# Performance work log

Hardware: AMD Instinct MI355X
Metric: run time of the kernel (lower is better)

The kernel has to match this reference:

```python
import jax, jax.numpy as jnp
import numpy as np

NV = 1_000_000   # number of 'var' nodes
NC = 500_000     # number of 'con' nodes
E = 16_000_000   # number of v2c edges (c2v is the reverse edge set)
H = 10           # n_h_feats


def setup_inputs() -> dict:
    key = jax.random.key(0)
    ks = jax.random.split(key, 24)
    s = 0.1  # weight init scale
    inp = {
        "var_c": jax.random.normal(ks[0], (NV,), jnp.float32),
        "var_x": jax.random.normal(ks[1], (NV,), jnp.float32),
        "con_b": jax.random.normal(ks[2], (NC,), jnp.float32),
        "A": jax.random.uniform(ks[3], (E,), jnp.float32),
        "src": jax.random.randint(ks[4], (E,), 0, NV, jnp.int32),
        "dst": jax.random.randint(ks[5], (E,), 0, NC, jnp.int32),
        # var_emb / con_emb Linear params
        "Wv": jax.random.normal(ks[6], (2, H), jnp.float32) * s,
        "bv": jnp.zeros((H,), jnp.float32),
        "Wc": jax.random.normal(ks[7], (1, H), jnp.float32) * s,
        "bc": jnp.zeros((H,), jnp.float32),
        # conv1 (GraphConv, shared across v2c/c2v) -- note: its output is
        # overwritten in the original forward and never reaches the output
        "W1": jax.random.normal(ks[8], (H, H), jnp.float32) * s,
        "b1": jnp.zeros((H,), jnp.float32),
        # conv2 (GraphConv, shared across v2c/c2v)
        "W2": jax.random.normal(ks[9], (H, H), jnp.float32) * s,
        "b2": jnp.zeros((H,), jnp.float32),
        # output MLP
        "Wo1": jax.random.normal(ks[10], (H, H), jnp.float32) * s,
        "bo1": jnp.zeros((H,), jnp.float32),
        "Wo2": jax.random.normal(ks[11], (H, H), jnp.float32) * s,
        "bo2": jnp.zeros((H,), jnp.float32),
        "Wo3": jax.random.normal(ks[12], (H, 1), jnp.float32) * s,
        "bo3": jnp.zeros((1,), jnp.float32),
    }
    return inp


def _gconv(x_src, W, b, s_idx, d_idx, ew, norm_src, norm_dst, n_dst):
    # DGL GraphConv, norm='both', with edge weights; in==out feats so W first.
    h = (x_src * norm_src) @ W                      # [N_src, H]
    msg = h[s_idx] * ew[:, None]                    # gather + edge weight
    agg = jax.ops.segment_sum(msg, d_idx, num_segments=n_dst)
    return agg * norm_dst + b


def reference(var_c, var_x, con_b, A, src, dst,
              Wv, bv, Wc, bc, W1, b1, W2, b2,
              Wo1, bo1, Wo2, bo2, Wo3, bo3):
    # symmetric norm from UNWEIGHTED degrees (DGL GraphConv norm='both'),
    # clamped at 1. v2c: out-deg(var), in-deg(con); c2v is the reverse.
    ones_e = jnp.ones_like(A)
    deg_v = jnp.clip(jax.ops.segment_sum(ones_e, src, num_segments=NV), 1.0)
    deg_c = jnp.clip(jax.ops.segment_sum(ones_e, dst, num_segments=NC), 1.0)
    norm_v = deg_v[:, None] ** -0.5
    norm_c = deg_c[:, None] ** -0.5

    # node embeddings
    var_feats = jnp.stack([var_c, var_x], axis=1)   # [NV, 2]
    X_var = jax.nn.relu(var_feats @ Wv + bv)        # [NV, H]
    X_con = jax.nn.relu(con_b[:, None] @ Wc + bc)   # [NC, H] (unused by convs: GraphConv ignores dst feats)

    # In the original forward, conv1 outputs (h_con / h_var) are immediately
    # overwritten by conv2 outputs (GraphConv only consumes src features),
    # so only conv2 lies on the effective compute path.
    h_con = jax.nn.relu(_gconv(X_var, W2, b2, src, dst, A, norm_v, norm_c, NC))
    h_var = jax.nn.relu(_gconv(h_con, W2, b2, dst, src, A, norm_c, norm_v, NV))

    h = jax.nn.relu(h_var @ Wo1 + bo1)
    h = jax.nn.relu(h @ Wo2 + bo2)
    logit = h @ Wo3 + bo3                           # [NV, 1]
    # dgl.readout_nodes(op='mean', ntype='var'), single graph -> [1, 1]
    return jnp.mean(logit, axis=0, keepdims=True)
```

## Files before the change

kernel.cpp:

```cpp
#include <hip/hip_runtime.h>

#define HF 10
#define ST 16
#define BST 16
#define SLC 256
#define NBINS 4096
#define NSL 16
#define CAPS 6144


__global__ __launch_bounds__(1024) void k_hist(const int* __restrict__ idx,
                                               unsigned* __restrict__ hist,
                                               long long s_begin, long long s_end, int per) {
    __shared__ unsigned l[NBINS];
    int t = threadIdx.x, sl = blockIdx.x;
    for (int b = t; b < NBINS; b += 1024) l[b] = 0u;
    __syncthreads();
    long long s0 = s_begin + (long long)sl * per;
    long long s1 = s0 + per; if (s1 > s_end) s1 = s_end;
    for (long long i = s0 + t; i < s1; i += 1024)
        atomicAdd(&l[((unsigned)idx[i]) >> 8], 1u);
    __syncthreads();
    unsigned* out = hist + (size_t)sl * NBINS;
    for (int b = t; b < NBINS; b += 1024) out[b] = l[b];
}

__global__ void k_coltot(const unsigned* __restrict__ h, unsigned* __restrict__ colT) {
    int b = blockIdx.x * 256 + threadIdx.x;
    unsigned s = 0u;
    for (int sl = 0; sl < SLC; sl++) s += h[(size_t)sl * NBINS + b];
    colT[b] = s;
}

__global__ __launch_bounds__(1024) void k_prefix(const unsigned* __restrict__ colT,
                                                 unsigned* __restrict__ start) {
    __shared__ unsigned p[1024];
    int t = threadIdx.x;
    uint4 v = *(const uint4*)(colT + 4 * t);
    unsigned own = v.x + v.y + v.z + v.w;
    p[t] = own;
    __syncthreads();
    for (int off = 1; off < 1024; off <<= 1) {
        unsigned u = (t >= off) ? p[t - off] : 0u;
        __syncthreads();
        p[t] += u;
        __syncthreads();
    }
    unsigned e = p[t] - own;
    *(uint4*)(start + 4 * t) = make_uint4(e, e + v.x, e + v.x + v.y, e + v.x + v.y + v.z);
    if (t == 1023) start[NBINS] = p[1023];
}

__global__ void k_offs(unsigned* __restrict__ h, const unsigned* __restrict__ start) {
    int b = blockIdx.x * 256 + threadIdx.x;
    unsigned cur = start[b];
    for (int sl = 0; sl < SLC; sl++) {
        unsigned* cell = h + (size_t)sl * NBINS + b;
        unsigned v = *cell;
        *cell = cur;
        cur += v;
    }
}

__global__ __launch_bounds__(1024) void k_scatS(const int* __restrict__ src, const int* __restrict__ dst,
                                                const float* __restrict__ A,
                                                const unsigned* __restrict__ offs,
                                                uint2* __restrict__ ebufS,
                                                long long E, int per) {
    __shared__ unsigned cur[NBINS];
    int t = threadIdx.x, sl = blockIdx.x;
    const unsigned* o = offs + (size_t)sl * NBINS;
    for (int b = t; b < NBINS; b += 1024) cur[b] = o[b];
    __syncthreads();
    long long s0 = (long long)sl * per;
    long long s1 = s0 + per; if (s1 > E) s1 = E;
    for (long long i = s0 + t; i < s1; i += 1024) {
        unsigned s = (unsigned)src[i], d = (unsigned)dst[i];
        float a = A[i];
        unsigned pos = atomicAdd(&cur[s >> 8], 1u);
        ebufS[pos] = make_uint2(((s & 255u) << 19) | d, __float_as_uint(a));
    }
}

__global__ __launch_bounds__(256) void k_sliceIP(uint2* __restrict__ ebuf,
                                                 const unsigned* __restrict__ startS) {
    __shared__ uint2 ebl[CAPS];
    __shared__ unsigned c16[NSL], p16[NSL];
    int t = threadIdx.x, b = blockIdx.x;
    unsigned i0 = startS[b], i1 = startS[b + 1], n = i1 - i0;
    if (n == 0u || n > (unsigned)CAPS) return;
    if (t < NSL) c16[t] = 0u;
    __syncthreads();
    for (unsigned i = t; i < n; i += 256) {
        uint2 kv = ebuf[i0 + i];
        ebl[i] = kv;
        atomicAdd(&c16[(kv.x & 0x7FFFFu) >> 15], 1u);
    }
    __syncthreads();
    if (t == 0) {
        unsigned run = 0u;
        for (int s = 0; s < NSL; s++) { p16[s] = run; run += c16[s]; }
    }
    __syncthreads();
    for (unsigned i = t; i < n; i += 256) {
        uint2 kv = ebl[i];
        unsigned pos = atomicAdd(&p16[(kv.x & 0x7FFFFu) >> 15], 1u);
        ebuf[i0 + pos] = kv;
    }
}

__global__ void k_cntS2(const uint2* __restrict__ ebufS, const unsigned* __restrict__ startS,
                        const float* __restrict__ var_c, const float* __restrict__ var_x,
                        float4* __restrict__ vcx, int NV) {
    __shared__ unsigned cnt[256];
    int t = threadIdx.x, b = blockIdx.x;
    cnt[t] = 0u;
    __syncthreads();
    unsigned i0 = startS[b], i1 = startS[b + 1];
    for (unsigned i = i0 + t; i < i1; i += 256)
        atomicAdd(&cnt[ebufS[i].x >> 19], 1u);
    __syncthreads();
    int v = b * 256 + t;
    if (v < NV)
        vcx[v] = make_float4(var_c[v], var_x[v], rsqrtf(fmaxf((float)cnt[t], 1.0f)), 0.0f);
}

__global__ __launch_bounds__(1024) void k_histD2(const uint2* __restrict__ ebufB,
                                                 const unsigned* __restrict__ startS,
                                                 unsigned* __restrict__ hist, int B0, int binsPer) {
    __shared__ unsigned l[NBINS];
    int t = threadIdx.x, sl = blockIdx.x;
    for (int b = t; b < NBINS; b += 1024) l[b] = 0u;
    __syncthreads();
    int b0 = B0 + sl * binsPer;
    unsigned i0 = startS[b0], i1 = startS[b0 + binsPer];
    for (unsigned i = i0 + t; i < i1; i += 1024)
        atomicAdd(&l[(ebufB[i].x & 0x7FFFFu) >> 8], 1u);
    __syncthreads();
    unsigned* out = hist + (size_t)sl * NBINS;
    for (int b = t; b < NBINS; b += 1024) out[b] = l[b];
}

__global__ __launch_bounds__(1024) void k_scatD2(const uint2* __restrict__ ebufB,
                                                 const unsigned* __restrict__ startS,
                                                 const unsigned* __restrict__ offs,
                                                 const float4* __restrict__ vcx,
                                                 uint4* __restrict__ ebufD, int B0, int binsPer,
                                                 unsigned cap) {
    __shared__ unsigned cur[NBINS];
    int t = threadIdx.x, sl = blockIdx.x;
    const unsigned* o = offs + (size_t)sl * NBINS;
    for (int b = t; b < NBINS; b += 1024) cur[b] = o[b];
    __syncthreads();
    int b0 = B0 + sl * binsPer;
    for (int bb = 0; bb < binsPer; bb++) {
        int bin = b0 + bb;
        unsigned vbase = ((unsigned)bin) << 8;
        unsigned i0 = startS[bin], i1 = startS[bin + 1];
        for (unsigned i = i0 + t; i < i1; i += 1024) {
            uint2 kv = ebufB[i];
            unsigned d = kv.x & 0x7FFFFu;
            float4 g = vcx[vbase | (kv.x >> 19)];
            unsigned pos = atomicAdd(&cur[d >> 8], 1u);
            if (pos < cap)
                ebufD[pos] = make_uint4(d & 255u, __float_as_uint(__uint_as_float(kv.y) * g.z),
                                        __float_as_uint(g.x), __float_as_uint(g.y));
        }
    }
}

__global__ __launch_bounds__(1024) void k_scatD(const int* __restrict__ src, const int* __restrict__ dst,
                                                const float* __restrict__ A,
                                                const unsigned* __restrict__ offs,
                                                const float4* __restrict__ vcx,
                                                uint4* __restrict__ ebufD,
                                                long long s_begin, long long s_end, int per) {
    __shared__ unsigned cur[NBINS];
    int t = threadIdx.x, sl = blockIdx.x;
    const unsigned* o = offs + (size_t)sl * NBINS;
    for (int b = t; b < NBINS; b += 1024) cur[b] = o[b];
    __syncthreads();
    long long s0 = s_begin + (long long)sl * per;
    long long s1 = s0 + per; if (s1 > s_end) s1 = s_end;
    for (long long i = s0 + t; i < s1; i += 4096) {
        unsigned sv[4], dv[4]; float av[4]; bool hv[4];
#pragma unroll
        for (int j = 0; j < 4; j++) {
            long long idx = i + (long long)j * 1024;
            hv[j] = idx < s1;
            if (hv[j]) { sv[j] = (unsigned)src[idx]; dv[j] = (unsigned)dst[idx]; av[j] = A[idx]; }
            else       { sv[j] = 0u; dv[j] = 0u; av[j] = 0.0f; }
        }
        float4 g[4];
#pragma unroll
        for (int j = 0; j < 4; j++)
            if (hv[j]) g[j] = vcx[sv[j]];
#pragma unroll
        for (int j = 0; j < 4; j++) {
            if (!hv[j]) continue;
            unsigned pos = atomicAdd(&cur[dv[j] >> 8], 1u);
            ebufD[pos] = make_uint4(dv[j] & 255u, __float_as_uint(av[j] * g[j].z),
                                    __float_as_uint(g[j].x), __float_as_uint(g[j].y));
        }
    }
}

__global__ void k_aggD(const uint4* __restrict__ ebufD, const unsigned* __restrict__ startD,
                       const float* __restrict__ Wv, const float* __restrict__ bv,
                       float* __restrict__ bufC, float* __restrict__ deg_c, int NC) {
    __shared__ float acc[256 * HF];
    __shared__ unsigned cnt[256];
    int t = threadIdx.x, b = blockIdx.x;
    for (int i = t; i < 256 * HF; i += 256) acc[i] = 0.0f;
    cnt[t] = 0u;
    float wv0[HF], wv1[HF], bvv[HF];
#pragma unroll
    for (int h = 0; h < HF; h++) { wv0[h] = Wv[h]; wv1[h] = Wv[HF + h]; bvv[h] = bv[h]; }
    __syncthreads();
    unsigned i0 = startD[b], i1 = startD[b + 1];
    for (unsigned i = i0 + t; i < i1; i += 256) {
        uint4 kv = ebufD[i];
        unsigned dl = kv.x;
        float anv = __uint_as_float(kv.y);
        float c   = __uint_as_float(kv.z);
        float x   = __uint_as_float(kv.w);
        float* ac = acc + dl * HF;
#pragma unroll
        for (int h = 0; h < HF; h++) {
            float e = fmaxf(fmaf(c, wv0[h], fmaf(x, wv1[h], bvv[h])), 0.0f);
            atomicAdd(ac + h, anv * e);
        }
        atomicAdd(&cnt[dl], 1u);
    }
    __syncthreads();
    int gid = b * 256 + t;
    if (gid < NC) {
        float* row = bufC + (size_t)gid * BST;
#pragma unroll
        for (int h = 0; h < HF; h++) row[h] += acc[t * HF + h];
        deg_c[gid] += (float)cnt[t];
    }
}

__global__ void k_conT(float* __restrict__ bufC, const float* __restrict__ deg_c,
                       const float* __restrict__ W2, const float* __restrict__ b2, int NC) {
    __shared__ float sW[HF * HF], sb[HF];
    int t = threadIdx.x;
    if (t < HF * HF) sW[t] = W2[t];
    if (t < HF)      sb[t] = b2[t];
    __syncthreads();
    int i = blockIdx.x * 256 + t;
    if (i >= NC) return;
    float nc = rsqrtf(fmaxf(deg_c[i], 1.0f));
    float* row = bufC + (size_t)i * BST;
    float x[HF];
#pragma unroll
    for (int h = 0; h < HF; h++) x[h] = row[h];
#pragma unroll
    for (int j = 0; j < HF; j++) {
        float a = 0.0f;
#pragma unroll
        for (int k = 0; k < HF; k++) a = fmaf(x[k], sW[k * HF + j], a);
        row[j] = fmaxf(fmaf(a, nc, sb[j]), 0.0f) * nc;
    }
}

__global__ void k_aggS(const uint2* __restrict__ ebufS, const unsigned* __restrict__ startS,
                       const float* __restrict__ bufC, const float4* __restrict__ vcx,
                       const float* __restrict__ W2, const float* __restrict__ b2,
                       const float* __restrict__ Wo1, const float* __restrict__ bo1,
                       const float* __restrict__ Wo2, const float* __restrict__ bo2,
                       const float* __restrict__ Wo3, const float* __restrict__ bo3,
                       double* __restrict__ gacc, int NV) {
    __shared__ float acc[256 * HF];
    __shared__ float sW2[HF * HF], sb2[HF], sW1[HF * HF], sb1[HF], sWm[HF * HF], sbm[HF], sW3[HF];
    __shared__ float sb3;
    __shared__ double red[256];
    int t = threadIdx.x, b = blockIdx.x;
    for (int i = t; i < 256 * HF; i += 256) acc[i] = 0.0f;
    if (t < HF * HF) { sW2[t] = W2[t]; sW1[t] = Wo1[t]; sWm[t] = Wo2[t]; }
    if (t < HF)      { sb2[t] = b2[t]; sb1[t] = bo1[t]; sbm[t] = bo2[t]; sW3[t] = Wo3[t]; }
    if (t == 0)      sb3 = bo3[0];
    __syncthreads();
    unsigned i0 = startS[b], i1 = startS[b + 1];
    int grp = t >> 2;
    int q   = t & 3;
    int nq  = (q < 2) ? 4 : (q == 2 ? 2 : 0);
    for (unsigned base = i0; base < i1; base += 64) {
        unsigned e = base + (unsigned)grp;
        bool ok = e < i1;
        uint2 kv = ok ? ebufS[e] : make_uint2(0u, 0u);
        float4 y = make_float4(0.f, 0.f, 0.f, 0.f);
        if (ok) y = *(const float4*)(bufC + (size_t)(kv.x & 0x7FFFFu) * BST + 4 * q);
        if (ok && nq) {
            float a = __uint_as_float(kv.y);
            float* ac = acc + (kv.x >> 19) * HF + 4 * q;
            atomicAdd(ac + 0, a * y.x);
            atomicAdd(ac + 1, a * y.y);
            if (nq == 4) {
                atomicAdd(ac + 2, a * y.z);
                atomicAdd(ac + 3, a * y.w);
            }
        }
    }
    __syncthreads();
    double local = 0.0;
    int v = b * 256 + t;
    if (v < NV) {
        float nv = vcx[v].z;
        float x[HF], hvv[HF], h1[HF], h2[HF];
#pragma unroll
        for (int h = 0; h < HF; h++) x[h] = acc[t * HF + h];
#pragma unroll
        for (int j = 0; j < HF; j++) {
            float a = 0.0f;
#pragma unroll
            for (int k = 0; k < HF; k++) a = fmaf(x[k], sW2[k * HF + j], a);
            hvv[j] = fmaxf(fmaf(a, nv, sb2[j]), 0.0f);
        }
#pragma unroll
        for (int j = 0; j < HF; j++) {
            float a = sb1[j];
#pragma unroll
            for (int k = 0; k < HF; k++) a = fmaf(hvv[k], sW1[k * HF + j], a);
            h1[j] = fmaxf(a, 0.0f);
        }
#pragma unroll
        for (int j = 0; j < HF; j++) {
            float a = sbm[j];
#pragma unroll
            for (int k = 0; k < HF; k++) a = fmaf(h1[k], sWm[k * HF + j], a);
            h2[j] = fmaxf(a, 0.0f);
        }
        float logit = sb3;
#pragma unroll
        for (int k = 0; k < HF; k++) logit = fmaf(h2[k], sW3[k], logit);
        local = (double)logit;
    }
    red[t] = local;
    __syncthreads();
    for (int s = 128; s > 0; s >>= 1) {
        if (t < s) red[t] += red[t + s];
        __syncthreads();
    }
    if (t == 0) atomicAdd(gacc, red[0]);
}

__global__ void k_out(const double* __restrict__ acc, float* __restrict__ out, int NV) {
    out[0] = (float)(acc[0] / (double)NV);
}


__global__ void k_degree(const int* __restrict__ src, const int* __restrict__ dst,
                         float* __restrict__ deg_v, float* __restrict__ deg_c, int E) {
    int i = blockIdx.x * blockDim.x + threadIdx.x;
    if (i < E) {
        atomicAdd(&deg_v[src[i]], 1.0f);
        atomicAdd(&deg_c[dst[i]], 1.0f);
    }
}

__global__ void k_norm(float* __restrict__ d, int n) {
    int i = blockIdx.x * blockDim.x + threadIdx.x;
    if (i < n) d[i] = 1.0f / sqrtf(fmaxf(d[i], 1.0f));
}

__global__ void k_var_emb(const float* __restrict__ var_c, const float* __restrict__ var_x,
                          const float* __restrict__ norm_v,
                          const float* __restrict__ Wv, const float* __restrict__ bv,
                          const float* __restrict__ W2,
                          float* __restrict__ out, int NV) {
    __shared__ float sWv[2 * HF], sbv[HF], sW2[HF * HF];
    int t = threadIdx.x;
    if (t < 2 * HF) sWv[t] = Wv[t];
    if (t < HF)     sbv[t] = bv[t];
    if (t < HF * HF) sW2[t] = W2[t];
    __syncthreads();
    int i = blockIdx.x * blockDim.x + t;
    if (i >= NV) return;
    float c = var_c[i], x = var_x[i], nv = norm_v[i];
    float e[HF];
#pragma unroll
    for (int h = 0; h < HF; h++)
        e[h] = fmaxf(fmaf(c, sWv[h], fmaf(x, sWv[HF + h], sbv[h])), 0.0f) * nv;
    float* row = out + (size_t)i * ST;
#pragma unroll
    for (int j = 0; j < HF; j++) {
        float acc = 0.0f;
#pragma unroll
        for (int k = 0; k < HF; k++) acc = fmaf(e[k], sW2[k * HF + j], acc);
        row[j] = acc;
    }
}

__global__ void k_edge(const int* __restrict__ gidx, const int* __restrict__ didx,
                       const float* __restrict__ A,
                       const float* __restrict__ h, float* __restrict__ agg, int E) {
    int tid = blockIdx.x * blockDim.x + threadIdx.x;
    int e = tid / 5;
    if (e >= E) return;
    int q = tid - e * 5;
    int s = gidx[e], d = didx[e];
    float a = A[e];
    const float2 m = *(const float2*)(h + (size_t)s * ST + 2 * q);
    float* o = agg + (size_t)d * ST + 2 * q;
    atomicAdd(o,     m.x * a);
    atomicAdd(o + 1, m.y * a);
}

__global__ void k_con(float* __restrict__ buf, const float* __restrict__ norm_c,
                      const float* __restrict__ W2, const float* __restrict__ b2, int NC) {
    __shared__ float sW2[HF * HF], sb2[HF];
    int t = threadIdx.x;
    if (t < HF * HF) sW2[t] = W2[t];
    if (t < HF)      sb2[t] = b2[t];
    __syncthreads();
    int i = blockIdx.x * blockDim.x + t;
    if (i >= NC) return;
    float nc = norm_c[i];
    float* row = buf + (size_t)i * ST;
    float hc[HF];
#pragma unroll
    for (int h = 0; h < HF; h++)
        hc[h] = fmaxf(fmaf(row[h], nc, sb2[h]), 0.0f) * nc;
#pragma unroll
    for (int j = 0; j < HF; j++) {
        float acc = 0.0f;
#pragma unroll
        for (int k = 0; k < HF; k++) acc = fmaf(hc[k], sW2[k * HF + j], acc);
        row[j] = acc;
    }
}

__global__ void k_final(const float* __restrict__ agg_v, const float* __restrict__ norm_v,
                        const float* __restrict__ b2,
                        const float* __restrict__ Wo1, const float* __restrict__ bo1,
                        const float* __restrict__ Wo2, const float* __restrict__ bo2,
                        const float* __restrict__ Wo3, const float* __restrict__ bo3,
                        double* __restrict__ acc, int NV) {
    __shared__ float sb2[HF], sW1[HF * HF], sb1[HF], sW2m[HF * HF], sb2m[HF], sW3[HF];
    __shared__ float sb3;
    __shared__ double red[256];
    int t = threadIdx.x;
    if (t < HF)      sb2[t]  = b2[t];
    if (t < HF * HF) sW1[t]  = Wo1[t];
    if (t < HF)      sb1[t]  = bo1[t];
    if (t < HF * HF) sW2m[t] = Wo2[t];
    if (t < HF)      sb2m[t] = bo2[t];
    if (t < HF)      sW3[t]  = Wo3[t];
    if (t == 0)      sb3     = bo3[0];
    __syncthreads();
    int i = blockIdx.x * blockDim.x + t;
    double local = 0.0;
    if (i < NV) {
        float nv = norm_v[i];
        const float* row = agg_v + (size_t)i * ST;
        float v[HF], h1[HF], h2[HF];
#pragma unroll
        for (int h = 0; h < HF; h++) v[h] = fmaxf(fmaf(row[h], nv, sb2[h]), 0.0f);
#pragma unroll
        for (int j = 0; j < HF; j++) {
            float a = sb1[j];
#pragma unroll
            for (int k = 0; k < HF; k++) a = fmaf(v[k], sW1[k * HF + j], a);
            h1[j] = fmaxf(a, 0.0f);
        }
#pragma unroll
        for (int j = 0; j < HF; j++) {
            float a = sb2m[j];
#pragma unroll
            for (int k = 0; k < HF; k++) a = fmaf(h1[k], sW2m[k * HF + j], a);
            h2[j] = fmaxf(a, 0.0f);
        }
        float logit = sb3;
#pragma unroll
        for (int k = 0; k < HF; k++) logit = fmaf(h2[k], sW3[k], logit);
        local = (double)logit;
    }
    red[t] = local;
    __syncthreads();
    for (int s = 128; s > 0; s >>= 1) {
        if (t < s) red[t] += red[t + s];
        __syncthreads();
    }
    if (t == 0) atomicAdd(acc, red[0]);
}


extern "C" void kernel_launch(void* const* d_in, const int* in_sizes, int n_in,
                              void* d_out, int out_size, void* d_ws, size_t ws_size,
                              hipStream_t stream) {
    const float* var_c = (const float*)d_in[0];
    const float* var_x = (const float*)d_in[1];
    const float* A   = (const float*)d_in[3];
    const int*   src = (const int*)d_in[4];
    const int*   dst = (const int*)d_in[5];
    const float* Wv  = (const float*)d_in[6];
    const float* bv  = (const float*)d_in[7];
    const float* W2  = (const float*)d_in[12];
    const float* b2  = (const float*)d_in[13];
    const float* Wo1 = (const float*)d_in[14];
    const float* bo1 = (const float*)d_in[15];
    const float* Wo2 = (const float*)d_in[16];
    const float* bo2 = (const float*)d_in[17];
    const float* Wo3 = (const float*)d_in[18];
    const float* bo3 = (const float*)d_in[19];

    const int NV = in_sizes[0];
    const int NC = in_sizes[2];
    const int E  = in_sizes[3];

    long long EcMaxUsed = 0;
    auto layout_bytes = [&](int nDc, bool binchunk, size_t* offs_out) -> size_t {
        size_t off = 0;
        auto alloc = [&](size_t bytes, int slot) {
            if (offs_out) offs_out[slot] = off;
            off = (off + bytes + 255) & ~(size_t)255;
        };
        long long ec;
        if (binchunk) {
            long long vspan = (long long)(NBINS / nDc) * 256;
            if (vspan > NV) vspan = NV;
            ec = ((long long)E * vspan) / NV + (long long)E / 64 + 1024;
            if (ec > E) ec = E;
        } else {
            ec = ((long long)E + nDc - 1) / nDc;
        }
        EcMaxUsed = ec;
        alloc((size_t)NC * BST * 4, 0);
        alloc((size_t)NV * 16, 1);
        alloc((size_t)NC * 4, 2);
        alloc((size_t)SLC * NBINS * 4, 3);
        alloc((size_t)SLC * NBINS * 4, 4);
        alloc((size_t)NBINS * 4, 5);
        alloc((size_t)(NBINS + 1) * 4, 6);
        alloc((size_t)(NBINS + 1) * 4, 7);
        alloc(8, 8);
        alloc((size_t)E * 8, 9);
        alloc((size_t)ec * 16, 10);
        return off;
    };

    int nD = 0;
    bool binc = false;
    size_t offs[11];
    for (int cand : {4, 8, 16}) {
        if (layout_bytes(cand, true, nullptr) <= ws_size) { nD = cand; binc = true; break; }
    }
    if (nD == 0) {
        for (int cand = 2; cand <= 16; cand++)
            if (layout_bytes(cand, false, nullptr) <= ws_size) { nD = cand; break; }
    }
    bool fast = (nD > 0) && (NV <= (1 << 20)) && (NC <= (1 << 19)) && (E > 0);

    char* ws = (char*)d_ws;
    if (fast) {
        layout_bytes(nD, binc, offs);
        const long long EcMax = EcMaxUsed;
        float*    bufC   = (float*)(ws + offs[0]);
        float4*   vcx    = (float4*)(ws + offs[1]);
        float*    deg_c  = (float*)(ws + offs[2]);
        unsigned* hS     = (unsigned*)(ws + offs[3]);
        unsigned* hD     = (unsigned*)(ws + offs[4]);
        unsigned* colT   = (unsigned*)(ws + offs[5]);
        unsigned* startS = (unsigned*)(ws + offs[6]);
        unsigned* startD = (unsigned*)(ws + offs[7]);
        double*   gacc   = (double*)(ws + offs[8]);
        uint2*    ebufS  = (uint2*)(ws + offs[9]);
        uint4*    ebufD  = (uint4*)(ws + offs[10]);

        const int perS = (int)(((long long)E + SLC - 1) / SLC);
        const int NB_S = (NV + 255) >> 8;
        const int NB_C = (NC + 255) >> 8;

        hipMemsetAsync(bufC,  0, (size_t)NC * BST * 4, stream);
        hipMemsetAsync(deg_c, 0, (size_t)NC * 4, stream);
        hipMemsetAsync(gacc,  0, 8, stream);

        k_hist<<<SLC, 1024, 0, stream>>>(src, hS, 0, E, perS);
        k_coltot<<<NBINS / 256, 256, 0, stream>>>(hS, colT);
        k_prefix<<<1, 1024, 0, stream>>>(colT, startS);
        k_offs<<<NBINS / 256, 256, 0, stream>>>(hS, startS);
        k_scatS<<<SLC, 1024, 0, stream>>>(src, dst, A, hS, ebufS, E, perS);

        k_sliceIP<<<NBINS, 256, 0, stream>>>(ebufS, startS);

        k_cntS2<<<NB_S, 256, 0, stream>>>(ebufS, startS, var_c, var_x, vcx, NV);

        if (binc) {
            const int binsChunk = NBINS / nD;
            const int binsPer   = binsChunk / SLC;
            for (int c = 0; c < nD; c++) {
                int B0 = c * binsChunk;
                k_histD2<<<SLC, 1024, 0, stream>>>(ebufS, startS, hD, B0, binsPer);
                k_coltot<<<NBINS / 256, 256, 0, stream>>>(hD, colT);
                k_prefix<<<1, 1024, 0, stream>>>(colT, startD);
                k_offs<<<NBINS / 256, 256, 0, stream>>>(hD, startD);
                k_scatD2<<<SLC, 1024, 0, stream>>>(ebufS, startS, hD, vcx, ebufD,
                                                   B0, binsPer, (unsigned)EcMax);
                k_aggD<<<NB_C, 256, 0, stream>>>(ebufD, startD, Wv, bv, bufC, deg_c, NC);
            }
        } else {
            const int perD = (int)((EcMax + SLC - 1) / SLC);
            for (int c = 0; c < nD; c++) {
                long long cb = (long long)c * EcMax;
                long long ce = cb + EcMax; if (ce > E) ce = E;
                k_hist<<<SLC, 1024, 0, stream>>>(dst, hD, cb, ce, perD);
                k_coltot<<<NBINS / 256, 256, 0, stream>>>(hD, colT);
                k_prefix<<<1, 1024, 0, stream>>>(colT, startD);
                k_offs<<<NBINS / 256, 256, 0, stream>>>(hD, startD);
                k_scatD<<<SLC, 1024, 0, stream>>>(src, dst, A, hD, vcx, ebufD, cb, ce, perD);
                k_aggD<<<NB_C, 256, 0, stream>>>(ebufD, startD, Wv, bv, bufC, deg_c, NC);
            }
        }
        k_conT<<<NB_C, 256, 0, stream>>>(bufC, deg_c, W2, b2, NC);

        k_aggS<<<NB_S, 256, 0, stream>>>(ebufS, startS, bufC, vcx, W2, b2,
                                         Wo1, bo1, Wo2, bo2, Wo3, bo3, gacc, NV);
        k_out<<<1, 1, 0, stream>>>(gacc, (float*)d_out, NV);
    } else {
        const int B = 256;
        float* fbufV = (float*)ws;
        float* fbufC = (float*)(ws + (size_t)NV * ST * 4);
        float* deg_v = (float*)(ws + (size_t)(NV + NC) * ST * 4);
        float* deg_c = deg_v + NV;
        size_t acc_off = ((size_t)(NV + NC) * ST * 4 + (size_t)(NV + NC) * 4 + 7) & ~(size_t)7;
        double* acc = (double*)(ws + acc_off);

        hipMemsetAsync(deg_v, 0, (size_t)(NV + NC) * 4, stream);
        hipMemsetAsync(fbufC, 0, (size_t)NC * ST * 4, stream);
        hipMemsetAsync(acc, 0, sizeof(double), stream);

        k_degree<<<(E + B - 1) / B, B, 0, stream>>>(src, dst, deg_v, deg_c, E);
        k_norm<<<(NV + NC + B - 1) / B, B, 0, stream>>>(deg_v, NV + NC);
        k_var_emb<<<(NV + B - 1) / B, B, 0, stream>>>(var_c, var_x, deg_v, Wv, bv, W2, fbufV, NV);

        long long tE = (long long)E * 5;
        k_edge<<<(int)((tE + B - 1) / B), B, 0, stream>>>(src, dst, A, fbufV, fbufC, E);
        k_con<<<(NC + B - 1) / B, B, 0, stream>>>(fbufC, deg_c, W2, b2, NC);

        hipMemsetAsync(fbufV, 0, (size_t)NV * ST * 4, stream);
        k_edge<<<(int)((tE + B - 1) / B), B, 0, stream>>>(dst, src, A, fbufC, fbufV, E);

        k_final<<<(NV + B - 1) / B, B, 0, stream>>>(fbufV, deg_v, b2, Wo1, bo1, Wo2, bo2, Wo3, bo3, acc, NV);
        k_out<<<1, 1, 0, stream>>>(acc, (float*)d_out, NV);
    }
}
```

Before: 2.722 ms.

## Sweep var-side aggregation by con-index slices with vectorized quad-lane gathers

k_sliceIP now records where each of the 16 con-index sub-slices starts inside every source bin. A new k_aggS2 kernel uses those offsets. Each block handles two source bins and walks the sub-slices in order, so concurrent blocks gather from a small window of bufC and stay cache-resident. Each edge is split across 4 lanes that read the con row with float4 loads and do the shared-memory atomics between them. The cost is an extra offset array and a fallback path for oversized bins, which are left unsorted and processed as a single slice.

```diff
diff --git a/kernel.cpp b/kernel.cpp
--- a/kernel.cpp
+++ b/kernel.cpp
@@ -7,6 +7,7 @@
 #define NBINS 4096
 #define NSL 16
 #define CAPS 6144
+#define BPB 2
 
 
 __global__ __launch_bounds__(1024) void k_hist(const int* __restrict__ idx,
@@ -83,12 +84,16 @@
 }
 
 __global__ __launch_bounds__(256) void k_sliceIP(uint2* __restrict__ ebuf,
-                                                 const unsigned* __restrict__ startS) {
+                                                 const unsigned* __restrict__ startS,
+                                                 unsigned* __restrict__ startS2) {
     __shared__ uint2 ebl[CAPS];
     __shared__ unsigned c16[NSL], p16[NSL];
     int t = threadIdx.x, b = blockIdx.x;
     unsigned i0 = startS[b], i1 = startS[b + 1], n = i1 - i0;
-    if (n == 0u || n > (unsigned)CAPS) return;
+    if (n > (unsigned)CAPS) {
+        if (t < NSL) startS2[b * NSL + t] = (t == 0) ? i0 : i1;
+        return;
+    }
     if (t < NSL) c16[t] = 0u;
     __syncthreads();
     for (unsigned i = t; i < n; i += 256) {
@@ -98,14 +103,14 @@
     }
     __syncthreads();
     if (t == 0) {
-        unsigned run = 0u;
-        for (int s = 0; s < NSL; s++) { p16[s] = run; run += c16[s]; }
+        unsigned run = i0;
+        for (int s = 0; s < NSL; s++) { p16[s] = run; startS2[b * NSL + s] = run; run += c16[s]; }
     }
     __syncthreads();
     for (unsigned i = t; i < n; i += 256) {
         uint2 kv = ebl[i];
         unsigned pos = atomicAdd(&p16[(kv.x & 0x7FFFFu) >> 15], 1u);
-        ebuf[i0 + pos] = kv;
+        ebuf[pos] = kv;
     }
 }
 
@@ -263,6 +268,102 @@
         for (int k = 0; k < HF; k++) a = fmaf(x[k], sW[k * HF + j], a);
         row[j] = fmaxf(fmaf(a, nc, sb[j]), 0.0f) * nc;
     }
+}
+
+__global__ __launch_bounds__(256) void k_aggS2(
+        const uint2* __restrict__ ebufS, const unsigned* __restrict__ startS,
+        const unsigned* __restrict__ startS2,
+        const float* __restrict__ bufC, const float4* __restrict__ vcx,
+        const float* __restrict__ W2, const float* __restrict__ b2,
+        const float* __restrict__ Wo1, const float* __restrict__ bo1,
+        const float* __restrict__ Wo2, const float* __restrict__ bo2,
+        const float* __restrict__ Wo3, const float* __restrict__ bo3,
+        double* __restrict__ gacc, int NV) {
+    __shared__ __align__(16) float acc[BPB * 256 * HF];
+    __shared__ float sW2[HF * HF], sb2[HF], sW1[HF * HF], sb1[HF], sWm[HF * HF], sbm[HF], sW3[HF];
+    __shared__ float sb3;
+    int t = threadIdx.x;
+    int b0 = blockIdx.x * BPB;
+    for (int i = t; i < BPB * 256 * HF; i += 256) acc[i] = 0.0f;
+    if (t < HF * HF) { sW2[t] = W2[t]; sW1[t] = Wo1[t]; sWm[t] = Wo2[t]; }
+    if (t < HF)      { sb2[t] = b2[t]; sb1[t] = bo1[t]; sbm[t] = bo2[t]; sW3[t] = Wo3[t]; }
+    if (t == 0)      sb3 = bo3[0];
+    __syncthreads();
+    int grp = t >> 2;
+    int q   = t & 3;
+    int nq  = (q < 2) ? 4 : (q == 2 ? 2 : 0);
+    for (int s = 0; s < NSL; s++) {
+#pragma unroll
+        for (int p = 0; p < BPB; p++) {
+            int b = b0 + p;
+            unsigned j0 = startS2[b * NSL + s];
+            unsigned j1 = (s == NSL - 1) ? startS[b + 1] : startS2[b * NSL + s + 1];
+            float* accb = acc + p * 256 * HF;
+            for (unsigned base = j0; base < j1; base += 64) {
+                unsigned e = base + (unsigned)grp;
+                bool ok = e < j1;
+                uint2 kv = ok ? ebufS[e] : make_uint2(0u, 0u);
+                float4 y = make_float4(0.f, 0.f, 0.f, 0.f);
+                if (ok) y = *(const float4*)(bufC + (size_t)(kv.x & 0x7FFFFu) * BST + 4 * q);
+                if (ok && nq) {
+                    float a = __uint_as_float(kv.y);
+                    float* ac = accb + (kv.x >> 19) * HF + 4 * q;
+                    atomicAdd(ac + 0, a * y.x);
+                    atomicAdd(ac + 1, a * y.y);
+                    if (nq == 4) {
+                        atomicAdd(ac + 2, a * y.z);
+                        atomicAdd(ac + 3, a * y.w);
+                    }
+                }
+            }
+        }
+    }
+    __syncthreads();
+    double local = 0.0;
+#pragma unroll
+    for (int p = 0; p < BPB; p++) {
+        int v = (b0 + p) * 256 + t;
+        if (v < NV) {
+            float nv = vcx[v].z;
+            float x[HF], hvv[HF], h1[HF], h2[HF];
+#pragma unroll
+            for (int h = 0; h < HF; h++) x[h] = acc[p * 256 * HF + t * HF + h];
+#pragma unroll
+            for (int j = 0; j < HF; j++) {
+                float a = 0.0f;
+#pragma unroll
+                for (int k = 0; k < HF; k++) a = fmaf(x[k], sW2[k * HF + j], a);
+                hvv[j] = fmaxf(fmaf(a, nv, sb2[j]), 0.0f);
+            }
+#pragma unroll
+            for (int j = 0; j < HF; j++) {
+                float a = sb1[j];
+#pragma unroll
+                for (int k = 0; k < HF; k++) a = fmaf(hvv[k], sW1[k * HF + j], a);
+                h1[j] = fmaxf(a, 0.0f);
+            }
+#pragma unroll
+            for (int j = 0; j < HF; j++) {
+                float a = sbm[j];
+#pragma unroll
+                for (int k = 0; k < HF; k++) a = fmaf(h1[k], sWm[k * HF + j], a);
+                h2[j] = fmaxf(a, 0.0f);
+            }
+            float logit = sb3;
+#pragma unroll
+            for (int k = 0; k < HF; k++) logit = fmaf(h2[k], sW3[k], logit);
+            local += (double)logit;
+        }
+    }
+    __syncthreads();
+    double* red = (double*)acc;
+    red[t] = local;
+    __syncthreads();
+    for (int s = 128; s > 0; s >>= 1) {
+        if (t < s) red[t] += red[t + s];
+        __syncthreads();
+    }
+    if (t == 0) atomicAdd(gacc, red[0]);
 }
 
 __global__ void k_aggS(const uint2* __restrict__ ebufS, const unsigned* __restrict__ startS,
@@ -337,13 +438,14 @@
         for (int k = 0; k < HF; k++) logit = fmaf(h2[k], sW3[k], logit);
         local = (double)logit;
     }
-    red[t] = local;
+    __shared__ double redl[256];
+    redl[t] = local;
     __syncthreads();
     for (int s = 128; s > 0; s >>= 1) {
-        if (t < s) red[t] += red[t + s];
+        if (t < s) redl[t] += redl[t + s];
         __syncthreads();
     }
-    if (t == 0) atomicAdd(gacc, red[0]);
+    if (t == 0) atomicAdd(gacc, redl[0]);
 }
 
 __global__ void k_out(const double* __restrict__ acc, float* __restrict__ out, int NV) {
@@ -538,12 +640,13 @@
         alloc(8, 8);
         alloc((size_t)E * 8, 9);
         alloc((size_t)ec * 16, 10);
+        alloc((size_t)NBINS * NSL * 4, 11);
         return off;
     };
 
     int nD = 0;
     bool binc = false;
-    size_t offs[11];
+    size_t offs[12];
     for (int cand : {4, 8, 16}) {
         if (layout_bytes(cand, true, nullptr) <= ws_size) { nD = cand; binc = true; break; }
     }
@@ -568,6 +671,7 @@
         double*   gacc   = (double*)(ws + offs[8]);
         uint2*    ebufS  = (uint2*)(ws + offs[9]);
         uint4*    ebufD  = (uint4*)(ws + offs[10]);
+        unsigned* startS2 = (unsigned*)(ws + offs[11]);
 
         const int perS = (int)(((long long)E + SLC - 1) / SLC);
         const int NB_S = (NV + 255) >> 8;
@@ -583,7 +687,7 @@
         k_offs<<<NBINS / 256, 256, 0, stream>>>(hS, startS);
         k_scatS<<<SLC, 1024, 0, stream>>>(src, dst, A, hS, ebufS, E, perS);
 
-        k_sliceIP<<<NBINS, 256, 0, stream>>>(ebufS, startS);
+        k_sliceIP<<<NBINS, 256, 0, stream>>>(ebufS, startS, startS2);
 
         k_cntS2<<<NB_S, 256, 0, stream>>>(ebufS, startS, var_c, var_x, vcx, NV);
 
@@ -615,8 +719,14 @@
         }
         k_conT<<<NB_C, 256, 0, stream>>>(bufC, deg_c, W2, b2, NC);
 
-        k_aggS<<<NB_S, 256, 0, stream>>>(ebufS, startS, bufC, vcx, W2, b2,
-                                         Wo1, bo1, Wo2, bo2, Wo3, bo3, gacc, NV);
+        if (binc) {
+            const int NBB = (NB_S + BPB - 1) / BPB;
+            k_aggS2<<<NBB, 256, 0, stream>>>(ebufS, startS, startS2, bufC, vcx, W2, b2,
+                                             Wo1, bo1, Wo2, bo2, Wo3, bo3, gacc, NV);
+        } else {
+            k_aggS<<<NB_S, 256, 0, stream>>>(ebufS, startS, bufC, vcx, W2, b2,
+                                             Wo1, bo1, Wo2, bo2, Wo3, bo3, gacc, NV);
+        }
         k_out<<<1, 1, 0, stream>>>(gacc, (float*)d_out, NV);
     } else {
         const int B = 256;
```

Result: no change. 2.739 ms (+0.6%).

## Tile-local LDS sort in source scatter, coarsen bins to 512 vertices, drop slice pass

Applied to the files above, without the earlier changes.

The source-side scatter now sorts each tile of 12288 edges by bin in shared memory, then writes contiguous runs per bin to global memory. This replaces per-edge random 8-byte global stores with mostly coalesced ones. Bins are widened to 512 vertices (2048 bins), and the count and aggregation kernels handle 512 vertices per block. The separate in-place dst-slice reorder pass is removed. That removes one full read/write of the edge buffer, but loses the dst-sorted order inside each bin that helped locality in the later dst scatter.

```diff
diff --git a/kernel.cpp b/kernel.cpp
--- a/kernel.cpp
+++ b/kernel.cpp
@@ -4,14 +4,15 @@
 #define ST 16
 #define BST 16
 #define SLC 256
-#define NBINS 4096
-#define NSL 16
-#define CAPS 6144
+#define NBINS 2048
+#define VPB 512
+#define TILE 12288
 
 
 __global__ __launch_bounds__(1024) void k_hist(const int* __restrict__ idx,
                                                unsigned* __restrict__ hist,
-                                               long long s_begin, long long s_end, int per) {
+                                               long long s_begin, long long s_end,
+                                               int per, int shift) {
     __shared__ unsigned l[NBINS];
     int t = threadIdx.x, sl = blockIdx.x;
     for (int b = t; b < NBINS; b += 1024) l[b] = 0u;
@@ -19,7 +20,7 @@
     long long s0 = s_begin + (long long)sl * per;
     long long s1 = s0 + per; if (s1 > s_end) s1 = s_end;
     for (long long i = s0 + t; i < s1; i += 1024)
-        atomicAdd(&l[((unsigned)idx[i]) >> 8], 1u);
+        atomicAdd(&l[((unsigned)idx[i]) >> shift], 1u);
     __syncthreads();
     unsigned* out = hist + (size_t)sl * NBINS;
     for (int b = t; b < NBINS; b += 1024) out[b] = l[b];
@@ -36,8 +37,8 @@
                                                  unsigned* __restrict__ start) {
     __shared__ unsigned p[1024];
     int t = threadIdx.x;
-    uint4 v = *(const uint4*)(colT + 4 * t);
-    unsigned own = v.x + v.y + v.z + v.w;
+    uint2 v = *(const uint2*)(colT + 2 * t);
+    unsigned own = v.x + v.y;
     p[t] = own;
     __syncthreads();
     for (int off = 1; off < 1024; off <<= 1) {
@@ -47,7 +48,7 @@
         __syncthreads();
     }
     unsigned e = p[t] - own;
-    *(uint4*)(start + 4 * t) = make_uint4(e, e + v.x, e + v.x + v.y, e + v.x + v.y + v.z);
+    *(uint2*)(start + 2 * t) = make_uint2(e, e + v.x);
     if (t == 1023) start[NBINS] = p[1023];
 }
 
@@ -62,67 +63,78 @@
     }
 }
 
-__global__ __launch_bounds__(1024) void k_scatS(const int* __restrict__ src, const int* __restrict__ dst,
-                                                const float* __restrict__ A,
-                                                const unsigned* __restrict__ offs,
-                                                uint2* __restrict__ ebufS,
-                                                long long E, int per) {
+__global__ __launch_bounds__(1024) void k_scatS2(
+        const int* __restrict__ src, const int* __restrict__ dst,
+        const float* __restrict__ A, const unsigned* __restrict__ offs,
+        uint2* __restrict__ ebufS, long long E, int per) {
     __shared__ unsigned cur[NBINS];
+    __shared__ unsigned th[NBINS];
+    __shared__ unsigned tf[NBINS];
+    __shared__ unsigned sc[1024];
+    __shared__ __align__(16) uint2 buf[TILE];
     int t = threadIdx.x, sl = blockIdx.x;
     const unsigned* o = offs + (size_t)sl * NBINS;
     for (int b = t; b < NBINS; b += 1024) cur[b] = o[b];
-    __syncthreads();
     long long s0 = (long long)sl * per;
     long long s1 = s0 + per; if (s1 > E) s1 = E;
-    for (long long i = s0 + t; i < s1; i += 1024) {
-        unsigned s = (unsigned)src[i], d = (unsigned)dst[i];
-        float a = A[i];
-        unsigned pos = atomicAdd(&cur[s >> 8], 1u);
-        ebufS[pos] = make_uint2(((s & 255u) << 19) | d, __float_as_uint(a));
-    }
-}
-
-__global__ __launch_bounds__(256) void k_sliceIP(uint2* __restrict__ ebuf,
-                                                 const unsigned* __restrict__ startS) {
-    __shared__ uint2 ebl[CAPS];
-    __shared__ unsigned c16[NSL], p16[NSL];
-    int t = threadIdx.x, b = blockIdx.x;
-    unsigned i0 = startS[b], i1 = startS[b + 1], n = i1 - i0;
-    if (n == 0u || n > (unsigned)CAPS) return;
-    if (t < NSL) c16[t] = 0u;
-    __syncthreads();
-    for (unsigned i = t; i < n; i += 256) {
-        uint2 kv = ebuf[i0 + i];
-        ebl[i] = kv;
-        atomicAdd(&c16[(kv.x & 0x7FFFFu) >> 15], 1u);
-    }
-    __syncthreads();
-    if (t == 0) {
-        unsigned run = 0u;
-        for (int s = 0; s < NSL; s++) { p16[s] = run; run += c16[s]; }
-    }
-    __syncthreads();
-    for (unsigned i = t; i < n; i += 256) {
-        uint2 kv = ebl[i];
-        unsigned pos = atomicAdd(&p16[(kv.x & 0x7FFFFu) >> 15], 1u);
-        ebuf[i0 + pos] = kv;
+    for (long long tb = s0; tb < s1; tb += TILE) {
+        int n = (int)((s1 - tb < (long long)TILE) ? (s1 - tb) : (long long)TILE);
+        for (int b = t; b < NBINS; b += 1024) th[b] = 0u;
+        __syncthreads();
+        for (int i = t; i < n; i += 1024)
+            atomicAdd(&th[((unsigned)src[tb + i]) >> 9], 1u);
+        __syncthreads();
+        unsigned a0 = th[2 * t], a1 = th[2 * t + 1];
+        unsigned own = a0 + a1;
+        sc[t] = own;
+        __syncthreads();
+        for (int off = 1; off < 1024; off <<= 1) {
+            unsigned u = (t >= off) ? sc[t - off] : 0u;
+            __syncthreads();
+            sc[t] += u;
+            __syncthreads();
+        }
+        unsigned ex = sc[t] - own;
+        th[2 * t] = ex;     th[2 * t + 1] = ex + a0;
+        tf[2 * t] = ex;     tf[2 * t + 1] = ex + a0;
+        __syncthreads();
+        for (int i = t; i < n; i += 1024) {
+            unsigned s = (unsigned)src[tb + i], d = (unsigned)dst[tb + i];
+            float a = A[tb + i];
+            unsigned p = atomicAdd(&tf[s >> 9], 1u);
+            buf[p] = make_uint2(((s & 511u) << 19) | d, __float_as_uint(a));
+        }
+        __syncthreads();
+        int w = t >> 6, ln = t & 63;
+        for (int b = w; b < NBINS; b += 16) {
+            unsigned lo = th[b], cnt = tf[b] - lo, gb = cur[b];
+            for (unsigned j = ln; j < cnt; j += 64)
+                ebufS[gb + j] = buf[lo + j];
+        }
+        __syncthreads();
+        for (int b = t; b < NBINS; b += 1024) cur[b] += tf[b] - th[b];
+        __syncthreads();
     }
 }
 
 __global__ void k_cntS2(const uint2* __restrict__ ebufS, const unsigned* __restrict__ startS,
                         const float* __restrict__ var_c, const float* __restrict__ var_x,
                         float4* __restrict__ vcx, int NV) {
-    __shared__ unsigned cnt[256];
+    __shared__ unsigned cnt[VPB];
     int t = threadIdx.x, b = blockIdx.x;
-    cnt[t] = 0u;
+    cnt[t] = 0u; cnt[t + 256] = 0u;
     __syncthreads();
     unsigned i0 = startS[b], i1 = startS[b + 1];
     for (unsigned i = i0 + t; i < i1; i += 256)
         atomicAdd(&cnt[ebufS[i].x >> 19], 1u);
     __syncthreads();
-    int v = b * 256 + t;
-    if (v < NV)
-        vcx[v] = make_float4(var_c[v], var_x[v], rsqrtf(fmaxf((float)cnt[t], 1.0f)), 0.0f);
+#pragma unroll
+    for (int k = 0; k < 2; k++) {
+        int v = b * VPB + k * 256 + t;
+        if (v < NV)
+            vcx[v] = make_float4(var_c[v], var_x[v],
+                                 rsqrtf(fmaxf((float)cnt[k * 256 + t], 1.0f)), 0.0f);
+    }
 }
 
 __global__ __launch_bounds__(1024) void k_histD2(const uint2* __restrict__ ebufB,
@@ -155,7 +167,7 @@
     int b0 = B0 + sl * binsPer;
     for (int bb = 0; bb < binsPer; bb++) {
         int bin = b0 + bb;
-        unsigned vbase = ((unsigned)bin) << 8;
+        unsigned vbase = ((unsigned)bin) << 9;
         unsigned i0 = startS[bin], i1 = startS[bin + 1];
         for (unsigned i = i0 + t; i < i1; i += 1024) {
             uint2 kv = ebufB[i];
@@ -265,19 +277,20 @@
     }
 }
 
-__global__ void k_aggS(const uint2* __restrict__ ebufS, const unsigned* __restrict__ startS,
-                       const float* __restrict__ bufC, const float4* __restrict__ vcx,
-                       const float* __restrict__ W2, const float* __restrict__ b2,
-                       const float* __restrict__ Wo1, const float* __restrict__ bo1,
-                       const float* __restrict__ Wo2, const float* __restrict__ bo2,
-                       const float* __restrict__ Wo3, const float* __restrict__ bo3,
-                       double* __restrict__ gacc, int NV) {
-    __shared__ float acc[256 * HF];
+__global__ __launch_bounds__(256) void k_aggS(
+        const uint2* __restrict__ ebufS, const unsigned* __restrict__ startS,
+        const float* __restrict__ bufC, const float4* __restrict__ vcx,
+        const float* __restrict__ W2, const float* __restrict__ b2,
+        const float* __restrict__ Wo1, const float* __restrict__ bo1,
+        const float* __restrict__ Wo2, const float* __restrict__ bo2,
+        const float* __restrict__ Wo3, const float* __restrict__ bo3,
+        double* __restrict__ gacc, int NV) {
+    __shared__ float acc[VPB * HF];
     __shared__ float sW2[HF * HF], sb2[HF], sW1[HF * HF], sb1[HF], sWm[HF * HF], sbm[HF], sW3[HF];
     __shared__ float sb3;
     __shared__ double red[256];
     int t = threadIdx.x, b = blockIdx.x;
-    for (int i = t; i < 256 * HF; i += 256) acc[i] = 0.0f;
+    for (int i = t; i < VPB * HF; i += 256) acc[i] = 0.0f;
     if (t < HF * HF) { sW2[t] = W2[t]; sW1[t] = Wo1[t]; sWm[t] = Wo2[t]; }
     if (t < HF)      { sb2[t] = b2[t]; sb1[t] = bo1[t]; sbm[t] = bo2[t]; sW3[t] = Wo3[t]; }
     if (t == 0)      sb3 = bo3[0];
@@ -305,37 +318,40 @@
     }
     __syncthreads();
     double local = 0.0;
-    int v = b * 256 + t;
-    if (v < NV) {
-        float nv = vcx[v].z;
-        float x[HF], hvv[HF], h1[HF], h2[HF];
-#pragma unroll
-        for (int h = 0; h < HF; h++) x[h] = acc[t * HF + h];
-#pragma unroll
-        for (int j = 0; j < HF; j++) {
-            float a = 0.0f;
-#pragma unroll
-            for (int k = 0; k < HF; k++) a = fmaf(x[k], sW2[k * HF + j], a);
-            hvv[j] = fmaxf(fmaf(a, nv, sb2[j]), 0.0f);
-        }
-#pragma unroll
-        for (int j = 0; j < HF; j++) {
-            float a = sb1[j];
-#pragma unroll
-            for (int k = 0; k < HF; k++) a = fmaf(hvv[k], sW1[k * HF + j], a);
-            h1[j] = fmaxf(a, 0.0f);
-        }
-#pragma unroll
-        for (int j = 0; j < HF; j++) {
-            float a = sbm[j];
-#pragma unroll
-            for (int k = 0; k < HF; k++) a = fmaf(h1[k], sWm[k * HF + j], a);
-            h2[j] = fmaxf(a, 0.0f);
-        }
-        float logit = sb3;
-#pragma unroll
-        for (int k = 0; k < HF; k++) logit = fmaf(h2[k], sW3[k], logit);
-        local = (double)logit;
+#pragma unroll
+    for (int k = 0; k < 2; k++) {
+        int v = b * VPB + k * 256 + t;
+        if (v < NV) {
+            float nv = vcx[v].z;
+            float x[HF], hvv[HF], h1[HF], h2[HF];
+#pragma unroll
+            for (int h = 0; h < HF; h++) x[h] = acc[(k * 256 + t) * HF + h];
+#pragma unroll
+            for (int j = 0; j < HF; j++) {
+                float a = 0.0f;
+#pragma unroll
+                for (int kk = 0; kk < HF; kk++) a = fmaf(x[kk], sW2[kk * HF + j], a);
+                hvv[j] = fmaxf(fmaf(a, nv, sb2[j]), 0.0f);
+            }
+#pragma unroll
+            for (int j = 0; j < HF; j++) {
+                float a = sb1[j];
+#pragma unroll
+                for (int kk = 0; kk < HF; kk++) a = fmaf(hvv[kk], sW1[kk * HF + j], a);
+                h1[j] = fmaxf(a, 0.0f);
+            }
+#pragma unroll
+            for (int j = 0; j < HF; j++) {
+                float a = sbm[j];
+#pragma unroll
+                for (int kk = 0; kk < HF; kk++) a = fmaf(h1[kk], sWm[kk * HF + j], a);
+                h2[j] = fmaxf(a, 0.0f);
+            }
+            float logit = sb3;
+#pragma unroll
+            for (int kk = 0; kk < HF; kk++) logit = fmaf(h2[kk], sW3[kk], logit);
+            local += (double)logit;
+        }
     }
     red[t] = local;
     __syncthreads();
@@ -519,7 +535,7 @@
         };
         long long ec;
         if (binchunk) {
-            long long vspan = (long long)(NBINS / nDc) * 256;
+            long long vspan = (long long)(NBINS / nDc) * VPB;
             if (vspan > NV) vspan = NV;
             ec = ((long long)E * vspan) / NV + (long long)E / 64 + 1024;
             if (ec > E) ec = E;
@@ -570,26 +586,24 @@
         uint4*    ebufD  = (uint4*)(ws + offs[10]);
 
         const int perS = (int)(((long long)E + SLC - 1) / SLC);
-        const int NB_S = (NV + 255) >> 8;
+        const int NB_S = (NV + VPB - 1) / VPB;
         const int NB_C = (NC + 255) >> 8;
 
         hipMemsetAsync(bufC,  0, (size_t)NC * BST * 4, stream);
         hipMemsetAsync(deg_c, 0, (size_t)NC * 4, stream);
         hipMemsetAsync(gacc,  0, 8, stream);
 
-        k_hist<<<SLC, 1024, 0, stream>>>(src, hS, 0, E, perS);
+        k_hist<<<SLC, 1024, 0, stream>>>(src, hS, 0, E, perS, 9);
         k_coltot<<<NBINS / 256, 256, 0, stream>>>(hS, colT);
         k_prefix<<<1, 1024, 0, stream>>>(colT, startS);
         k_offs<<<NBINS / 256, 256, 0, stream>>>(hS, startS);
-        k_scatS<<<SLC, 1024, 0, stream>>>(src, dst, A, hS, ebufS, E, perS);
-
-        k_sliceIP<<<NBINS, 256, 0, stream>>>(ebufS, startS);
+        k_scatS2<<<SLC, 1024, 0, stream>>>(src, dst, A, hS, ebufS, E, perS);
 
         k_cntS2<<<NB_S, 256, 0, stream>>>(ebufS, startS, var_c, var_x, vcx, NV);
 
         if (binc) {
             const int binsChunk = NBINS / nD;
-            const int binsPer   = binsChunk / SLC;
+            const int binsPer   = (binsChunk + SLC - 1) / SLC;
             for (int c = 0; c < nD; c++) {
                 int B0 = c * binsChunk;
                 k_histD2<<<SLC, 1024, 0, stream>>>(ebufS, startS, hD, B0, binsPer);
@@ -605,7 +619,7 @@
             for (int c = 0; c < nD; c++) {
                 long long cb = (long long)c * EcMax;
                 long long ce = cb + EcMax; if (ce > E) ce = E;
-                k_hist<<<SLC, 1024, 0, stream>>>(dst, hD, cb, ce, perD);
+                k_hist<<<SLC, 1024, 0, stream>>>(dst, hD, cb, ce, perD, 8);
                 k_coltot<<<NBINS / 256, 256, 0, stream>>>(hD, colT);
                 k_prefix<<<1, 1024, 0, stream>>>(colT, startD);
                 k_offs<<<NBINS / 256, 256, 0, stream>>>(hD, startD);
```

Measured after the change: 2.533 ms. 1.07x faster.
